# Kernel optimization log

Hardware: AMD Instinct MI355X
Metric: run time of the kernel (lower is better)

Reference implementation:

```python
import jax, jax.numpy as jnp
import numpy as np

HIDDEN = 4096
NUM_HEADS = 32
HEAD_DIM = HIDDEN // NUM_HEADS  # 128
ROPE_THETA = 10000.0
B, S = 1, 2048


def setup_inputs() -> dict:
    key = jax.random.key(0)
    k1, k2, k3, k4 = jax.random.split(key, 4)
    positions = jnp.broadcast_to(jnp.arange(S, dtype=jnp.int32), (B, S))
    hidden_states = jax.random.normal(k1, (B, S, HIDDEN), dtype=jnp.float32)
    # fused QKV projection (bias=True), output projection (bias=False)
    w_qkv = jax.random.normal(k2, (HIDDEN, 3 * HIDDEN), dtype=jnp.float32) * (HIDDEN ** -0.5)
    b_qkv = jax.random.normal(k3, (3 * HIDDEN,), dtype=jnp.float32) * 0.01
    w_o = jax.random.normal(k4, (HIDDEN, HIDDEN), dtype=jnp.float32) * (HIDDEN ** -0.5)
    return {"positions": positions, "hidden_states": hidden_states,
            "w_qkv": w_qkv, "b_qkv": b_qkv, "w_o": w_o}


def _apply_rope(x, positions):
    # x: [B, S, N, D]; NeoX-style rotate-half RoPE, rotary_dim == head_dim
    half = HEAD_DIM // 2
    inv_freq = 1.0 / (ROPE_THETA ** (jnp.arange(0, half, dtype=jnp.float32) / half))
    angles = positions.astype(jnp.float32)[..., None] * inv_freq  # [B, S, half]
    cos = jnp.cos(angles)[:, :, None, :]  # [B, S, 1, half]
    sin = jnp.sin(angles)[:, :, None, :]
    x1, x2 = x[..., :half], x[..., half:]
    return jnp.concatenate([x1 * cos - x2 * sin, x2 * cos + x1 * sin], axis=-1)


def reference(positions, hidden_states, w_qkv, b_qkv, w_o):
    qkv = jnp.einsum('bsh,hd->bsd', hidden_states, w_qkv) + b_qkv  # [B, S, 3H]
    q, k, v = jnp.split(qkv, 3, axis=-1)
    q = q.reshape(B, S, NUM_HEADS, HEAD_DIM)
    k = k.reshape(B, S, NUM_HEADS, HEAD_DIM)
    v = v.reshape(B, S, NUM_HEADS, HEAD_DIM)
    q = _apply_rope(q, positions)
    k = _apply_rope(k, positions)
    scale = HEAD_DIM ** -0.5
    scores = jnp.einsum('bqnd,bknd->bnqk', q, k) * scale  # [B, N, S, S]
    causal = jnp.tril(jnp.ones((S, S), dtype=bool))
    scores = jnp.where(causal, scores, jnp.finfo(scores.dtype).min)
    probs = jax.nn.softmax(scores, axis=-1)
    attn = jnp.einsum('bnqk,bknd->bqnd', probs, v).reshape(B, S, HIDDEN)
    return jnp.einsum('bsh,ho->bso', attn, w_o)
```

## Files before the change

### kernel.cpp

```cpp
#include <hip/hip_runtime.h>
#include <hip/hip_bf16.h>

#define S_LEN 2048
#define HID   4096
#define NH    32
#define HD    128
#define KD    4096

typedef __attribute__((ext_vector_type(4))) float f32x4;
typedef __attribute__((ext_vector_type(8))) short s16x8;
typedef __attribute__((ext_vector_type(4))) short s16x4;

#define AS1 __attribute__((address_space(1)))
#define AS3 __attribute__((address_space(3)))

__device__ __forceinline__ void gl_lds16(const void* g, void* l) {
  __builtin_amdgcn_global_load_lds((const AS1 void*)g, (AS3 void*)l, 16, 0, 0);
}

__device__ inline short f2bf(float f) {
  union { float f; unsigned u; } v; v.f = f;
  return (short)((v.u + 0x7fffu + ((v.u >> 16) & 1u)) >> 16);
}
__device__ inline float bf2f(short s) {
  union { unsigned u; float f; } v; v.u = ((unsigned)(unsigned short)s) << 16;
  return v.f;
}
__device__ inline unsigned packbf(float a, float b) {
  return (unsigned)(unsigned short)f2bf(a) | ((unsigned)(unsigned short)f2bf(b) << 16);
}

__global__ __launch_bounds__(256)
void cvt_kernel(const float* __restrict__ A, short* __restrict__ Ab) {
  const size_t i = ((size_t)blockIdx.x * 256 + threadIdx.x) * 8;
  f32x4 v0 = *(const f32x4*)&A[i];
  f32x4 v1 = *(const f32x4*)&A[i + 4];
  s16x8 r;
  r[0]=f2bf(v0[0]); r[1]=f2bf(v0[1]); r[2]=f2bf(v0[2]); r[3]=f2bf(v0[3]);
  r[4]=f2bf(v1[0]); r[5]=f2bf(v1[1]); r[6]=f2bf(v1[2]); r[7]=f2bf(v1[3]);
  *(s16x8*)&Ab[i] = r;
}

__global__ __launch_bounds__(256)
void transcvt_kernel(const float* __restrict__ W, short* __restrict__ Wt, const int N) {
  __shared__ float tile[64][65];
  const int k0 = blockIdx.x * 64, n0 = blockIdx.y * 64;
  const int t = threadIdx.x;
#pragma unroll
  for (int i = 0; i < 16; ++i) {
    const int e = i * 256 + t;
    const int k = e >> 6, n = e & 63;
    tile[n][k] = W[(size_t)(k0 + k) * N + n0 + n];
  }
  __syncthreads();
  const int nn = t >> 2, ks = (t & 3) * 16;
  s16x8 a, b;
#pragma unroll
  for (int i = 0; i < 8; i++) a[i] = f2bf(tile[nn][ks + i]);
#pragma unroll
  for (int i = 0; i < 8; i++) b[i] = f2bf(tile[nn][ks + 8 + i]);
  *(s16x8*)&Wt[(size_t)(n0 + nn) * KD + k0 + ks]     = a;
  *(s16x8*)&Wt[(size_t)(n0 + nn) * KD + k0 + ks + 8] = b;
}

template<int EPI>
__global__ __launch_bounds__(256, 2)
void gemm5_kernel(const short* __restrict__ A, const short* __restrict__ Bt,
                  const float* __restrict__ bias,
                  short* __restrict__ Qb, short* __restrict__ Kb, short* __restrict__ Vb,
                  float* __restrict__ Cout)
{
  __shared__ char sm[3][24576] __attribute__((aligned(128)));
  const int KD2 = KD * 2;
  const int bid = blockIdx.x;
  const int xcd = bid & 7, idx = bid >> 3;
  const int m0 = (idx & 7) * 256;
  const int n0 = (xcd * ((EPI == 0) ? 12 : 4) + (idx >> 3)) * 128;

  const int t = threadIdx.x, lane = t & 63, c = lane & 15, g = lane >> 4;
  const int w = t >> 6, wr = w >> 1, wc = w & 1;
  const int flip = ((c >> 1) & 7) << 4;
  const int laneA = wr * 8192 + ((c * 64 + g * 16) ^ flip);
  const int laneB = 16384 + wc * 4096 + ((c * 64 + g * 16) ^ flip);

  const char* srcA[4];
  const char* srcB[2];
#pragma unroll
  for (int j = 0; j < 4; ++j) {
    const int la = j * 4096 + t * 16;
    const int ls = la ^ ((la >> 3) & 0x70);
    srcA[j] = (const char*)A + (size_t)(m0 + (ls >> 6)) * KD2 + (ls & 63);
  }
#pragma unroll
  for (int j = 0; j < 2; ++j) {
    const int la = j * 4096 + t * 16;
    const int ls = la ^ ((la >> 3) & 0x70);
    srcB[j] = (const char*)Bt + (size_t)(n0 + (ls >> 6)) * KD2 + (ls & 63);
  }

  f32x4 acc[8][4];
#pragma unroll
  for (int i = 0; i < 8; i++)
#pragma unroll
    for (int j = 0; j < 4; j++) acc[i][j] = (f32x4){0.f, 0.f, 0.f, 0.f};

#define STG(S, H) do {                                        \
    const size_t ko_ = (size_t)(H) * 64;                      \
    gl_lds16(srcA[0] + ko_, sm[S] + t * 16);                  \
    gl_lds16(srcA[1] + ko_, sm[S] + 4096  + t * 16);          \
    gl_lds16(srcA[2] + ko_, sm[S] + 8192  + t * 16);          \
    gl_lds16(srcA[3] + ko_, sm[S] + 12288 + t * 16);          \
    gl_lds16(srcB[0] + ko_, sm[S] + 16384 + t * 16);          \
    gl_lds16(srcB[1] + ko_, sm[S] + 20480 + t * 16);          \
  } while (0)

#define COMP(S) do {                                                       \
    const char* b_ = sm[S];                                                \
    s16x8 a_[8], bb_[4];                                                   \
    _Pragma("unroll")                                                      \
    for (int mi = 0; mi < 8; ++mi) a_[mi] = *(const s16x8*)(b_ + laneA + mi * 1024); \
    _Pragma("unroll")                                                      \
    for (int ni = 0; ni < 4; ++ni) bb_[ni] = *(const s16x8*)(b_ + laneB + ni * 1024); \
    __builtin_amdgcn_s_setprio(1);                                         \
    _Pragma("unroll")                                                      \
    for (int mi = 0; mi < 8; ++mi)                                         \
      _Pragma("unroll")                                                    \
      for (int ni = 0; ni < 4; ++ni)                                       \
        acc[mi][ni] = __builtin_amdgcn_mfma_f32_16x16x32_bf16(a_[mi], bb_[ni], acc[mi][ni], 0, 0, 0); \
    __builtin_amdgcn_s_setprio(0);                                         \
  } while (0)

#define WAIT6 asm volatile("s_waitcnt vmcnt(6)" ::: "memory")
#define WAIT0 asm volatile("s_waitcnt vmcnt(0)" ::: "memory")
#define BARR  do { __builtin_amdgcn_s_barrier(); asm volatile("" ::: "memory"); } while (0)

  STG(0, 0); STG(1, 1);
  for (int j = 0; j < 42; ++j) {
    const int h = 3 * j;
    WAIT6; BARR; STG(2, h + 2); COMP(0);
    WAIT6; BARR; STG(0, h + 3); COMP(1);
    WAIT6; BARR; STG(1, h + 4); COMP(2);
  }
  WAIT6; BARR; COMP(0);
  WAIT0; BARR; COMP(1);

#undef STG
#undef COMP
#undef WAIT6
#undef WAIT0
#undef BARR

  if (EPI == 0) {
#pragma unroll
    for (int ni = 0; ni < 4; ++ni) {
      const int ncol = n0 + wc * 64 + ni * 16 + c;
      const int which = ncol >> 12;
      const int h = (ncol >> 7) & 31;
      const int dcl = ncol & 127;
      short* dst = (which == 0) ? Qb : ((which == 1) ? Kb : Vb);
      const float bv = bias[ncol];
#pragma unroll
      for (int mi = 0; mi < 8; ++mi)
#pragma unroll
        for (int jj = 0; jj < 4; ++jj) {
          const int row = m0 + wr * 128 + mi * 16 + g * 4 + jj;
          dst[((size_t)h * S_LEN + row) * HD + dcl] = f2bf(acc[mi][ni][jj] + bv);
        }
    }
  } else {
#pragma unroll
    for (int ni = 0; ni < 4; ++ni) {
      const int ncol = n0 + wc * 64 + ni * 16 + c;
#pragma unroll
      for (int mi = 0; mi < 8; ++mi)
#pragma unroll
        for (int jj = 0; jj < 4; ++jj) {
          const int row = m0 + wr * 128 + mi * 16 + g * 4 + jj;
          Cout[(size_t)row * HID + ncol] = acc[mi][ni][jj];
        }
    }
  }
}

__global__ __launch_bounds__(256, 3)
void gemm7_kernel(const short* __restrict__ A, const short* __restrict__ Bt,
                  float* __restrict__ Cout)
{
  __shared__ char sm[3][16384] __attribute__((aligned(128)));
  const int KD2 = KD * 2;
  const int bid = blockIdx.x;
  const int xcd = bid & 7, idx = bid >> 3;
  const int m0 = (idx & 15) * 128;
  const int n0 = (xcd * 4 + (idx >> 4)) * 128;

  const int t = threadIdx.x, lane = t & 63, c = lane & 15, g = lane >> 4;
  const int w = t >> 6, wr = w >> 1, wc = w & 1;
  const int flip = ((c >> 1) & 7) << 4;
  const int laneA = wr * 4096 + ((c * 64 + g * 16) ^ flip);
  const int laneB = 8192 + wc * 4096 + ((c * 64 + g * 16) ^ flip);

  const char* srcA[2];
  const char* srcB[2];
#pragma unroll
  for (int j = 0; j < 2; ++j) {
    const int la = j * 4096 + t * 16;
    const int ls = la ^ ((la >> 3) & 0x70);
    srcA[j] = (const char*)A  + (size_t)(m0 + (ls >> 6)) * KD2 + (ls & 63);
    srcB[j] = (const char*)Bt + (size_t)(n0 + (ls >> 6)) * KD2 + (ls & 63);
  }

  f32x4 acc[4][4];
#pragma unroll
  for (int i = 0; i < 4; i++)
#pragma unroll
    for (int j = 0; j < 4; j++) acc[i][j] = (f32x4){0.f, 0.f, 0.f, 0.f};

#define STG7(S, H) do {                                       \
    const size_t ko_ = (size_t)(H) * 64;                      \
    gl_lds16(srcA[0] + ko_, sm[S] + t * 16);                  \
    gl_lds16(srcA[1] + ko_, sm[S] + 4096  + t * 16);          \
    gl_lds16(srcB[0] + ko_, sm[S] + 8192  + t * 16);          \
    gl_lds16(srcB[1] + ko_, sm[S] + 12288 + t * 16);          \
  } while (0)

#define COMP7(S) do {                                                      \
    const char* b_ = sm[S];                                                \
    s16x8 a_[4], bb_[4];                                                   \
    _Pragma("unroll")                                                      \
    for (int mi = 0; mi < 4; ++mi) a_[mi] = *(const s16x8*)(b_ + laneA + mi * 1024); \
    _Pragma("unroll")                                                      \
    for (int ni = 0; ni < 4; ++ni) bb_[ni] = *(const s16x8*)(b_ + laneB + ni * 1024); \
    __builtin_amdgcn_s_setprio(1);                                         \
    _Pragma("unroll")                                                      \
    for (int mi = 0; mi < 4; ++mi)                                         \
      _Pragma("unroll")                                                    \
      for (int ni = 0; ni < 4; ++ni)                                       \
        acc[mi][ni] = __builtin_amdgcn_mfma_f32_16x16x32_bf16(a_[mi], bb_[ni], acc[mi][ni], 0, 0, 0); \
    __builtin_amdgcn_s_setprio(0);                                         \
  } while (0)

#define WAIT4 asm volatile("s_waitcnt vmcnt(4)" ::: "memory")
#define WAIT0 asm volatile("s_waitcnt vmcnt(0)" ::: "memory")
#define BARR  do { __builtin_amdgcn_s_barrier(); asm volatile("" ::: "memory"); } while (0)

  STG7(0, 0); STG7(1, 1);
  for (int j = 0; j < 42; ++j) {
    const int h = 3 * j;
    WAIT4; BARR; STG7(2, h + 2); COMP7(0);
    WAIT4; BARR; STG7(0, h + 3); COMP7(1);
    WAIT4; BARR; STG7(1, h + 4); COMP7(2);
  }
  WAIT4; BARR; COMP7(0);
  WAIT0; BARR; COMP7(1);

#undef STG7
#undef COMP7
#undef WAIT4
#undef WAIT0
#undef BARR

#pragma unroll
  for (int ni = 0; ni < 4; ++ni) {
    const int ncol = n0 + wc * 64 + ni * 16 + c;
#pragma unroll
    for (int mi = 0; mi < 4; ++mi)
#pragma unroll
      for (int jj = 0; jj < 4; ++jj) {
        const int row = m0 + wr * 64 + mi * 16 + g * 4 + jj;
        Cout[(size_t)row * HID + ncol] = acc[mi][ni][jj];
      }
  }
}

template<int EPI, int ABF16>
__global__ __launch_bounds__(256)
void gemm_kernel(const void* __restrict__ Av, const float* __restrict__ B,
                 const float* __restrict__ bias, const int N,
                 short* __restrict__ Qb, short* __restrict__ Kb, short* __restrict__ Vb,
                 float* __restrict__ Cout)
{
  __shared__ short As[128][40];
  __shared__ short Bs[128][40];
  const int m0 = blockIdx.x * 128;
  const int nb = blockIdx.y * 128;
  const int t  = threadIdx.x;
  const int w = t >> 6, lane = t & 63, c = lane & 15, g = lane >> 4;
  const int wm = (w >> 1) * 64, wn = (w & 1) * 64;

  f32x4 acc[4][4];
#pragma unroll
  for (int i = 0; i < 4; i++)
#pragma unroll
    for (int j = 0; j < 4; j++) acc[i][j] = (f32x4){0.f, 0.f, 0.f, 0.f};

  const int ar = t >> 3;
  const int ac = (t & 7) * 4;
  const int bn = t & 127;
  const int bkq = (t >> 7) * 16;

  for (int k0 = 0; k0 < KD; k0 += 32) {
#pragma unroll
    for (int rr = 0; rr < 4; rr++) {
      const int row = rr * 32 + ar;
      if (ABF16) {
        *(s16x4*)&As[row][ac] =
          *(const s16x4*)((const short*)Av + (size_t)(m0 + row) * KD + k0 + ac);
      } else {
        f32x4 v = *(const f32x4*)((const float*)Av + (size_t)(m0 + row) * KD + k0 + ac);
        s16x4 pk;
        pk[0] = f2bf(v[0]); pk[1] = f2bf(v[1]); pk[2] = f2bf(v[2]); pk[3] = f2bf(v[3]);
        *(s16x4*)&As[row][ac] = pk;
      }
    }
    const float* pB = B + (size_t)(k0 + bkq) * N + nb + bn;
    s16x8 b0, b1;
#pragma unroll
    for (int i = 0; i < 8; i++) b0[i] = f2bf(pB[(size_t)i * N]);
#pragma unroll
    for (int i = 0; i < 8; i++) b1[i] = f2bf(pB[(size_t)(i + 8) * N]);
    *(s16x8*)&Bs[bn][bkq]     = b0;
    *(s16x8*)&Bs[bn][bkq + 8] = b1;
    __syncthreads();
    s16x8 af[4], bfr[4];
#pragma unroll
    for (int i = 0; i < 4; i++) af[i]  = *(const s16x8*)&As[wm + i * 16 + c][g * 8];
#pragma unroll
    for (int i = 0; i < 4; i++) bfr[i] = *(const s16x8*)&Bs[wn + i * 16 + c][g * 8];
#pragma unroll
    for (int mi = 0; mi < 4; mi++)
#pragma unroll
      for (int ni = 0; ni < 4; ni++)
        acc[mi][ni] = __builtin_amdgcn_mfma_f32_16x16x32_bf16(af[mi], bfr[ni], acc[mi][ni], 0, 0, 0);
    __syncthreads();
  }

  if (EPI == 0) {
    const int which = nb >> 12;
    const int h = (nb & 4095) >> 7;
    short* dst = (which == 0) ? Qb : ((which == 1) ? Kb : Vb);
#pragma unroll
    for (int ni = 0; ni < 4; ni++) {
      const int d = wn + ni * 16 + c;
      const float bv = bias[nb + d];
#pragma unroll
      for (int mi = 0; mi < 4; mi++)
#pragma unroll
        for (int j = 0; j < 4; j++) {
          const int row = m0 + wm + mi * 16 + g * 4 + j;
          dst[((size_t)h * S_LEN + row) * HD + d] = f2bf(acc[mi][ni][j] + bv);
        }
    }
  } else {
#pragma unroll
    for (int ni = 0; ni < 4; ni++) {
      const int n = nb + wn + ni * 16 + c;
#pragma unroll
      for (int mi = 0; mi < 4; mi++)
#pragma unroll
        for (int j = 0; j < 4; j++) {
          const int row = m0 + wm + mi * 16 + g * 4 + j;
          Cout[(size_t)row * N + n] = acc[mi][ni][j];
        }
    }
  }
}

__global__ void rope_kernel(const int* __restrict__ positions,
                            short* __restrict__ Qb, short* __restrict__ Kb)
{
  const int s = blockIdx.x;
  const int h = blockIdx.y * 4 + threadIdx.y;
  const int d = threadIdx.x;
  const float pos = (float)positions[s];
  const float inv_freq = exp2f(-(float)d * 0.20762050593046014f);
  const float ang = pos * inv_freq;
  float sn, cs;
  sincosf(ang, &sn, &cs);
  const size_t base = ((size_t)h * S_LEN + s) * HD + d;
  const float scale = 0.08838834764831845f;
  float x1 = bf2f(Qb[base]), x2 = bf2f(Qb[base + 64]);
  Qb[base]      = f2bf((x1 * cs - x2 * sn) * scale);
  Qb[base + 64] = f2bf((x2 * cs + x1 * sn) * scale);
  x1 = bf2f(Kb[base]); x2 = bf2f(Kb[base + 64]);
  Kb[base]      = f2bf(x1 * cs - x2 * sn);
  Kb[base + 64] = f2bf(x2 * cs + x1 * sn);
}

__global__ __launch_bounds__(256)
void vtrans_kernel(const short* __restrict__ V, short* __restrict__ Vt)
{
  __shared__ short tile[64][72];
  const int h = blockIdx.z;
  const int s0 = blockIdx.x * 64;
  const int d0 = blockIdx.y * 64;
  const int tx = threadIdx.x & 63, ty = threadIdx.x >> 6;
  for (int r = ty; r < 64; r += 4)
    tile[r][tx] = V[((size_t)h * S_LEN + s0 + r) * HD + d0 + tx];
  __syncthreads();
  for (int r = ty; r < 64; r += 4)
    Vt[((size_t)h * HD + d0 + r) * S_LEN + s0 + tx] = tile[tx][r];
}

__global__ __launch_bounds__(512)
void attn_kernel(const short* __restrict__ Q, const short* __restrict__ Kg,
                 const short* __restrict__ Vtg, short* __restrict__ attn_out)
{
  __shared__ short Ks[2][64][128];
  __shared__ short Vs[2][128][72];
  const int h = blockIdx.y;
  const int ib = blockIdx.x;
  const int q0a = ib * 128;
  const int q0b = (15 - ib) * 128;
  const int nt0 = 2 * ib + 2;
  const int nt1 = 32 - 2 * ib;
  const int t = threadIdx.x;
  const int w = t >> 6, lane = t & 63, c = lane & 15, g = lane >> 4;
  const short* Qh = Q   + (size_t)h * S_LEN * HD;
  const short* Kh = Kg  + (size_t)h * S_LEN * HD;
  const short* Vh = Vtg + (size_t)h * HD * S_LEN;

  const int krow = t >> 4, kch = t & 15;
  const int vrow = t >> 3, vch = t & 7;
  const int ksw = (kch ^ ((krow & 3) | ((krow >> 1) & 4))) * 16;

  const int rbase = (c >> 2) * 8 + (c & 3);
  const int sb = (rbase & 3) | ((rbase >> 1) & 4);
  int koff[4];
#pragma unroll
  for (int di = 0; di < 4; ++di) koff[di] = ((di * 4 + g) ^ sb) * 16;

  const int qga = q0a + w * 16 + c;
  const int qgb = q0b + w * 16 + c;
  s16x8 qfa[4], qfb[4];
#pragma unroll
  for (int di = 0; di < 4; di++) {
    qfa[di] = *(const s16x8*)&Qh[(size_t)qga * HD + di * 32 + g * 8];
    qfb[di] = *(const s16x8*)&Qh[(size_t)qgb * HD + di * 32 + g * 8];
  }

  f32x4 oa[8], ob[8];
#pragma unroll
  for (int dt = 0; dt < 8; dt++) {
    oa[dt] = (f32x4){0.f, 0.f, 0.f, 0.f};
    ob[dt] = (f32x4){0.f, 0.f, 0.f, 0.f};
  }
  float m_a = -3.0e38f, l_a = 0.f, m_b = -3.0e38f, l_b = 0.f;

#define SM_PANEL(SA, SB, SC, SD, QG, FULL, MR, LR, OARR, PB0, PB1) do {        \
    float v_[16];                                                              \
    if (FULL) {                                                                \
      _Pragma("unroll")                                                        \
      for (int j = 0; j < 4; ++j) {                                            \
        v_[j] = SA[j]; v_[4 + j] = SB[j]; v_[8 + j] = SC[j]; v_[12 + j] = SD[j]; \
      }                                                                        \
    } else {                                                                   \
      _Pragma("unroll")                                                        \
      for (int j = 0; j < 4; ++j) {                                            \
        v_[j]      = (kb + 8 * g + j          <= (QG)) ? SA[j] : -__builtin_inff(); \
        v_[4 + j]  = (kb + 8 * g + 4 + j      <= (QG)) ? SB[j] : -__builtin_inff(); \
        v_[8 + j]  = (kb + 32 + 8 * g + j     <= (QG)) ? SC[j] : -__builtin_inff(); \
        v_[12 + j] = (kb + 32 + 8 * g + 4 + j <= (QG)) ? SD[j] : -__builtin_inff(); \
      }                                                                        \
    }                                                                          \
    float mx_ = v_[0];                                                         \
    _Pragma("unroll")                                                          \
    for (int ii = 1; ii < 16; ++ii) mx_ = fmaxf(mx_, v_[ii]);                  \
    mx_ = fmaxf(mx_, __shfl_xor(mx_, 16, 64));                                 \
    mx_ = fmaxf(mx_, __shfl_xor(mx_, 32, 64));                                 \
    const float mn_ = fmaxf(MR, mx_);                                          \
    if (!__all(mn_ - MR <= 8.0f)) {                                            \
      const float al_ = __expf(MR - mn_);                                      \
      LR *= al_;                                                               \
      _Pragma("unroll")                                                        \
      for (int dt = 0; dt < 8; ++dt)                                           \
        _Pragma("unroll")                                                      \
        for (int j = 0; j < 4; ++j) OARR[dt][j] *= al_;                        \
      MR = mn_;                                                                \
    }                                                                          \
    float p_[16], rs_ = 0.f;                                                   \
    _Pragma("unroll")                                                          \
    for (int ii = 0; ii < 16; ++ii) { p_[ii] = __expf(v_[ii] - MR); rs_ += p_[ii]; } \
    rs_ += __shfl_xor(rs_, 16, 64);                                            \
    rs_ += __shfl_xor(rs_, 32, 64);                                            \
    LR += rs_;                                                                 \
    union { s16x8 v8; unsigned u[4]; } pu0_, pu1_;                             \
    pu0_.u[0] = packbf(p_[0], p_[1]);   pu0_.u[1] = packbf(p_[2], p_[3]);      \
    pu0_.u[2] = packbf(p_[4], p_[5]);   pu0_.u[3] = packbf(p_[6], p_[7]);      \
    pu1_.u[0] = packbf(p_[8], p_[9]);   pu1_.u[1] = packbf(p_[10], p_[11]);    \
    pu1_.u[2] = packbf(p_[12], p_[13]); pu1_.u[3] = packbf(p_[14], p_[15]);    \
    PB0 = pu0_.v8; PB1 = pu1_.v8;                                              \
  } while (0)

  {
#pragma unroll
    for (int i = 0; i < 2; ++i) {
      s16x8 gK = *(const s16x8*)&Kh[(size_t)(i * 32 + krow) * HD + kch * 8];
      s16x8 gV = *(const s16x8*)&Vh[(size_t)(i * 64 + vrow) * S_LEN + vch * 8];
      *(s16x8*)((char*)&Ks[0][0][0] + (i * 32 + krow) * 256 + ksw) = gK;
      *(s16x8*)&Vs[0][i * 64 + vrow][vch * 8] = gV;
    }
  }
  __syncthreads();

  for (int kt = 0; kt < nt1; kt++) {
    const int cur = kt & 1;
    const int kb = kt * 64;
    const bool do0 = (kt < nt0);
    s16x8 gK0, gK1, gV0, gV1;
    if (kt + 1 < nt1) {
      gK0 = *(const s16x8*)&Kh[(size_t)(kb + 64 + krow) * HD + kch * 8];
      gK1 = *(const s16x8*)&Kh[(size_t)(kb + 96 + krow) * HD + kch * 8];
      gV0 = *(const s16x8*)&Vh[(size_t)vrow * S_LEN + kb + 64 + vch * 8];
      gV1 = *(const s16x8*)&Vh[(size_t)(64 + vrow) * S_LEN + kb + 64 + vch * 8];
    }
    f32x4 bA = (f32x4){0,0,0,0}, bB = (f32x4){0,0,0,0};
    f32x4 bC = (f32x4){0,0,0,0}, bD = (f32x4){0,0,0,0};
    f32x4 aA = (f32x4){0,0,0,0}, aB = (f32x4){0,0,0,0};
    f32x4 aC = (f32x4){0,0,0,0}, aD = (f32x4){0,0,0,0};
    const char* kbase = (const char*)&Ks[cur][0][0] + rbase * 256;
    __builtin_amdgcn_s_setprio(1);
    if (do0) {
#pragma unroll
      for (int di = 0; di < 4; ++di) {
        const char* p = kbase + koff[di];
        s16x8 kA = *(const s16x8*)(p);
        s16x8 kB = *(const s16x8*)(p + 1024);
        s16x8 kC = *(const s16x8*)(p + 8192);
        s16x8 kD = *(const s16x8*)(p + 9216);
        bA = __builtin_amdgcn_mfma_f32_16x16x32_bf16(kA, qfb[di], bA, 0, 0, 0);
        bB = __builtin_amdgcn_mfma_f32_16x16x32_bf16(kB, qfb[di], bB, 0, 0, 0);
        bC = __builtin_amdgcn_mfma_f32_16x16x32_bf16(kC, qfb[di], bC, 0, 0, 0);
        bD = __builtin_amdgcn_mfma_f32_16x16x32_bf16(kD, qfb[di], bD, 0, 0, 0);
        aA = __builtin_amdgcn_mfma_f32_16x16x32_bf16(kA, qfa[di], aA, 0, 0, 0);
        aB = __builtin_amdgcn_mfma_f32_16x16x32_bf16(kB, qfa[di], aB, 0, 0, 0);
        aC = __builtin_amdgcn_mfma_f32_16x16x32_bf16(kC, qfa[di], aC, 0, 0, 0);
        aD = __builtin_amdgcn_mfma_f32_16x16x32_bf16(kD, qfa[di], aD, 0, 0, 0);
      }
    } else {
#pragma unroll
      for (int di = 0; di < 4; ++di) {
        const char* p = kbase + koff[di];
        s16x8 kA = *(const s16x8*)(p);
        s16x8 kB = *(const s16x8*)(p + 1024);
        s16x8 kC = *(const s16x8*)(p + 8192);
        s16x8 kD = *(const s16x8*)(p + 9216);
        bA = __builtin_amdgcn_mfma_f32_16x16x32_bf16(kA, qfb[di], bA, 0, 0, 0);
        bB = __builtin_amdgcn_mfma_f32_16x16x32_bf16(kB, qfb[di], bB, 0, 0, 0);
        bC = __builtin_amdgcn_mfma_f32_16x16x32_bf16(kC, qfb[di], bC, 0, 0, 0);
        bD = __builtin_amdgcn_mfma_f32_16x16x32_bf16(kD, qfb[di], bD, 0, 0, 0);
      }
    }
    __builtin_amdgcn_s_setprio(0);
    s16x8 pb0, pb1, pa0, pa1;
    const bool fullb = (kb + 64 <= q0b);
    SM_PANEL(bA, bB, bC, bD, qgb, fullb, m_b, l_b, ob, pb0, pb1);
    if (do0) {
      const bool fulla = (kb + 64 <= q0a);
      SM_PANEL(aA, aB, aC, aD, qga, fulla, m_a, l_a, oa, pa0, pa1);
    }
    __builtin_amdgcn_s_setprio(1);
    if (do0) {
#pragma unroll
      for (int dt = 0; dt < 8; dt++) {
        s16x8 vf0 = *(const s16x8*)&Vs[cur][dt * 16 + c][g * 8];
        s16x8 vf1 = *(const s16x8*)&Vs[cur][dt * 16 + c][32 + g * 8];
        ob[dt] = __builtin_amdgcn_mfma_f32_16x16x32_bf16(vf0, pb0, ob[dt], 0, 0, 0);
        ob[dt] = __builtin_amdgcn_mfma_f32_16x16x32_bf16(vf1, pb1, ob[dt], 0, 0, 0);
        oa[dt] = __builtin_amdgcn_mfma_f32_16x16x32_bf16(vf0, pa0, oa[dt], 0, 0, 0);
        oa[dt] = __builtin_amdgcn_mfma_f32_16x16x32_bf16(vf1, pa1, oa[dt], 0, 0, 0);
      }
    } else {
#pragma unroll
      for (int dt = 0; dt < 8; dt++) {
        s16x8 vf0 = *(const s16x8*)&Vs[cur][dt * 16 + c][g * 8];
        s16x8 vf1 = *(const s16x8*)&Vs[cur][dt * 16 + c][32 + g * 8];
        ob[dt] = __builtin_amdgcn_mfma_f32_16x16x32_bf16(vf0, pb0, ob[dt], 0, 0, 0);
        ob[dt] = __builtin_amdgcn_mfma_f32_16x16x32_bf16(vf1, pb1, ob[dt], 0, 0, 0);
      }
    }
    __builtin_amdgcn_s_setprio(0);
    __syncthreads();
    if (kt + 1 < nt1) {
      *(s16x8*)((char*)&Ks[cur ^ 1][0][0] + krow * 256 + ksw)        = gK0;
      *(s16x8*)((char*)&Ks[cur ^ 1][0][0] + (32 + krow) * 256 + ksw) = gK1;
      *(s16x8*)&Vs[cur ^ 1][vrow][vch * 8]      = gV0;
      *(s16x8*)&Vs[cur ^ 1][64 + vrow][vch * 8] = gV1;
    }
    __syncthreads();
  }
#undef SM_PANEL

  const float inv_b = 1.0f / l_b;
  const float inv_a = 1.0f / l_a;
#pragma unroll
  for (int dt = 0; dt < 8; dt++) {
    s16x4 pkb, pka;
#pragma unroll
    for (int j = 0; j < 4; j++) {
      pkb[j] = f2bf(ob[dt][j] * inv_b);
      pka[j] = f2bf(oa[dt][j] * inv_a);
    }
    *(s16x4*)&attn_out[(size_t)qgb * HID + h * HD + dt * 16 + g * 4] = pkb;
    *(s16x4*)&attn_out[(size_t)qga * HID + h * HD + dt * 16 + g * 4] = pka;
  }
}

extern "C" void kernel_launch(void* const* d_in, const int* in_sizes, int n_in,
                              void* d_out, int out_size, void* d_ws, size_t ws_size,
                              hipStream_t stream)
{
  const int*   positions = (const int*)d_in[0];
  const float* hidden    = (const float*)d_in[1];
  const float* w_qkv     = (const float*)d_in[2];
  const float* b_qkv     = (const float*)d_in[3];
  const float* w_o       = (const float*)d_in[4];
  float* out = (float*)d_out;

  char* ws = (char*)d_ws;
  const size_t MB = (size_t)1 << 20;

  if (ws_size >= 224 * MB) {
    short* Ah    = (short*)(ws);
    short* Wqt   = (short*)(ws + 16 * MB);
    short* Wot   = (short*)(ws + 112 * MB);
    short* Qb    = (short*)(ws + 144 * MB);
    short* Kb    = (short*)(ws + 160 * MB);
    short* Vb    = (short*)(ws + 176 * MB);
    short* Vt    = (short*)(ws + 192 * MB);
    short* attnb = (short*)(ws + 208 * MB);

    cvt_kernel<<<4096, 256, 0, stream>>>(hidden, Ah);
    transcvt_kernel<<<dim3(KD / 64, 3 * HID / 64), 256, 0, stream>>>(w_qkv, Wqt, 3 * HID);
    transcvt_kernel<<<dim3(KD / 64, HID / 64), 256, 0, stream>>>(w_o, Wot, HID);
    gemm5_kernel<0><<<768, 256, 0, stream>>>(Ah, Wqt, b_qkv, Qb, Kb, Vb, nullptr);
    rope_kernel<<<dim3(S_LEN, NH / 4), dim3(64, 4), 0, stream>>>(positions, Qb, Kb);
    vtrans_kernel<<<dim3(S_LEN / 64, HD / 64, NH), 256, 0, stream>>>(Vb, Vt);
    attn_kernel<<<dim3(8, NH), 512, 0, stream>>>(Qb, Kb, Vt, attnb);
    gemm7_kernel<<<512, 256, 0, stream>>>(attnb, Wot, out);
  } else {
    short* Qb    = (short*)(ws);
    short* Kb    = (short*)(ws + 16 * MB);
    short* Vb    = (short*)(ws + 32 * MB);
    short* Vt    = (short*)(ws + 48 * MB);
    short* attnb = (short*)(ws + 64 * MB);

    gemm_kernel<0, 0><<<dim3(16, 96), 256, 0, stream>>>(hidden, w_qkv, b_qkv, 3 * HID,
                                                        Qb, Kb, Vb, nullptr);
    rope_kernel<<<dim3(S_LEN, NH / 4), dim3(64, 4), 0, stream>>>(positions, Qb, Kb);
    vtrans_kernel<<<dim3(S_LEN / 64, HD / 64, NH), 256, 0, stream>>>(Vb, Vt);
    attn_kernel<<<dim3(8, NH), 512, 0, stream>>>(Qb, Kb, Vt, attnb);
    gemm_kernel<1, 1><<<dim3(16, 32), 256, 0, stream>>>(attnb, w_o, nullptr, HID,
                                                        nullptr, nullptr, nullptr, out);
  }
}
```

Before: 469.8 us.

## Split GEMM k-step into two half-phases with interleaved staging and barriers

```diff
diff --git a/kernel.cpp b/kernel.cpp
--- a/kernel.cpp
+++ b/kernel.cpp
@@ -65,7 +65,7 @@
 
 template<int EPI>
 __global__ __launch_bounds__(256, 2)
-void gemm5_kernel(const short* __restrict__ A, const short* __restrict__ Bt,
+void gemm8_kernel(const short* __restrict__ A, const short* __restrict__ Bt,
                   const float* __restrict__ bias,
                   short* __restrict__ Qb, short* __restrict__ Kb, short* __restrict__ Vb,
                   float* __restrict__ Cout)
@@ -104,51 +104,66 @@
 #pragma unroll
     for (int j = 0; j < 4; j++) acc[i][j] = (f32x4){0.f, 0.f, 0.f, 0.f};
 
-#define STG(S, H) do {                                        \
+#define STG_H1(S, H) do {                                     \
     const size_t ko_ = (size_t)(H) * 64;                      \
     gl_lds16(srcA[0] + ko_, sm[S] + t * 16);                  \
     gl_lds16(srcA[1] + ko_, sm[S] + 4096  + t * 16);          \
     gl_lds16(srcA[2] + ko_, sm[S] + 8192  + t * 16);          \
+  } while (0)
+#define STG_H2(S, H) do {                                     \
+    const size_t ko_ = (size_t)(H) * 64;                      \
     gl_lds16(srcA[3] + ko_, sm[S] + 12288 + t * 16);          \
     gl_lds16(srcB[0] + ko_, sm[S] + 16384 + t * 16);          \
     gl_lds16(srcB[1] + ko_, sm[S] + 20480 + t * 16);          \
   } while (0)
 
-#define COMP(S) do {                                                       \
+#define TILE8(S, S2, H, DOSTG, WN) do {                                    \
+    asm volatile("s_waitcnt vmcnt(" #WN ")" ::: "memory");                 \
+    __builtin_amdgcn_s_barrier();                                          \
+    if (DOSTG) STG_H1(S2, H);                                              \
     const char* b_ = sm[S];                                                \
-    s16x8 a_[8], bb_[4];                                                   \
+    s16x8 al_[4], bb_[4];                                                  \
     _Pragma("unroll")                                                      \
-    for (int mi = 0; mi < 8; ++mi) a_[mi] = *(const s16x8*)(b_ + laneA + mi * 1024); \
+    for (int mi = 0; mi < 4; ++mi) al_[mi] = *(const s16x8*)(b_ + laneA + mi * 1024); \
     _Pragma("unroll")                                                      \
     for (int ni = 0; ni < 4; ++ni) bb_[ni] = *(const s16x8*)(b_ + laneB + ni * 1024); \
+    __builtin_amdgcn_s_barrier();                                          \
     __builtin_amdgcn_s_setprio(1);                                         \
     _Pragma("unroll")                                                      \
-    for (int mi = 0; mi < 8; ++mi)                                         \
+    for (int mi = 0; mi < 4; ++mi)                                         \
       _Pragma("unroll")                                                    \
       for (int ni = 0; ni < 4; ++ni)                                       \
-        acc[mi][ni] = __builtin_amdgcn_mfma_f32_16x16x32_bf16(a_[mi], bb_[ni], acc[mi][ni], 0, 0, 0); \
+        acc[mi][ni] = __builtin_amdgcn_mfma_f32_16x16x32_bf16(al_[mi], bb_[ni], acc[mi][ni], 0, 0, 0); \
+    __builtin_amdgcn_s_setprio(0);                                         \
+    __builtin_amdgcn_s_barrier();                                          \
+    if (DOSTG) STG_H2(S2, H);                                              \
+    s16x8 ah_[4];                                                          \
+    _Pragma("unroll")                                                      \
+    for (int mi = 0; mi < 4; ++mi) ah_[mi] = *(const s16x8*)(b_ + laneA + (4 + mi) * 1024); \
+    __builtin_amdgcn_s_barrier();                                          \
+    __builtin_amdgcn_s_setprio(1);                                         \
+    _Pragma("unroll")                                                      \
+    for (int mi = 0; mi < 4; ++mi)                                         \
+      _Pragma("unroll")                                                    \
+      for (int ni = 0; ni < 4; ++ni)                                       \
+        acc[4 + mi][ni] = __builtin_amdgcn_mfma_f32_16x16x32_bf16(ah_[mi], bb_[ni], acc[4 + mi][ni], 0, 0, 0); \
     __builtin_amdgcn_s_setprio(0);                                         \
   } while (0)
 
-#define WAIT6 asm volatile("s_waitcnt vmcnt(6)" ::: "memory")
-#define WAIT0 asm volatile("s_waitcnt vmcnt(0)" ::: "memory")
-#define BARR  do { __builtin_amdgcn_s_barrier(); asm volatile("" ::: "memory"); } while (0)
-
-  STG(0, 0); STG(1, 1);
+  STG_H1(0, 0); STG_H2(0, 0);
+  STG_H1(1, 1); STG_H2(1, 1);
   for (int j = 0; j < 42; ++j) {
     const int h = 3 * j;
-    WAIT6; BARR; STG(2, h + 2); COMP(0);
-    WAIT6; BARR; STG(0, h + 3); COMP(1);
-    WAIT6; BARR; STG(1, h + 4); COMP(2);
-  }
-  WAIT6; BARR; COMP(0);
-  WAIT0; BARR; COMP(1);
-
-#undef STG
-#undef COMP
-#undef WAIT6
-#undef WAIT0
-#undef BARR
+    TILE8(0, 2, h + 2, true, 6);
+    TILE8(1, 0, h + 3, true, 6);
+    TILE8(2, 1, h + 4, true, 6);
+  }
+  TILE8(0, 0, 0, false, 6);
+  TILE8(1, 0, 0, false, 0);
+
+#undef STG_H1
+#undef STG_H2
+#undef TILE8
 
   if (EPI == 0) {
 #pragma unroll
@@ -179,96 +194,6 @@
           Cout[(size_t)row * HID + ncol] = acc[mi][ni][jj];
         }
     }
-  }
-}
-
-__global__ __launch_bounds__(256, 3)
-void gemm7_kernel(const short* __restrict__ A, const short* __restrict__ Bt,
-                  float* __restrict__ Cout)
-{
-  __shared__ char sm[3][16384] __attribute__((aligned(128)));
-  const int KD2 = KD * 2;
-  const int bid = blockIdx.x;
-  const int xcd = bid & 7, idx = bid >> 3;
-  const int m0 = (idx & 15) * 128;
-  const int n0 = (xcd * 4 + (idx >> 4)) * 128;
-
-  const int t = threadIdx.x, lane = t & 63, c = lane & 15, g = lane >> 4;
-  const int w = t >> 6, wr = w >> 1, wc = w & 1;
-  const int flip = ((c >> 1) & 7) << 4;
-  const int laneA = wr * 4096 + ((c * 64 + g * 16) ^ flip);
-  const int laneB = 8192 + wc * 4096 + ((c * 64 + g * 16) ^ flip);
-
-  const char* srcA[2];
-  const char* srcB[2];
-#pragma unroll
-  for (int j = 0; j < 2; ++j) {
-    const int la = j * 4096 + t * 16;
-    const int ls = la ^ ((la >> 3) & 0x70);
-    srcA[j] = (const char*)A  + (size_t)(m0 + (ls >> 6)) * KD2 + (ls & 63);
-    srcB[j] = (const char*)Bt + (size_t)(n0 + (ls >> 6)) * KD2 + (ls & 63);
-  }
-
-  f32x4 acc[4][4];
-#pragma unroll
-  for (int i = 0; i < 4; i++)
-#pragma unroll
-    for (int j = 0; j < 4; j++) acc[i][j] = (f32x4){0.f, 0.f, 0.f, 0.f};
-
-#define STG7(S, H) do {                                       \
-    const size_t ko_ = (size_t)(H) * 64;                      \
-    gl_lds16(srcA[0] + ko_, sm[S] + t * 16);                  \
-    gl_lds16(srcA[1] + ko_, sm[S] + 4096  + t * 16);          \
-    gl_lds16(srcB[0] + ko_, sm[S] + 8192  + t * 16);          \
-    gl_lds16(srcB[1] + ko_, sm[S] + 12288 + t * 16);          \
-  } while (0)
-
-#define COMP7(S) do {                                                      \
-    const char* b_ = sm[S];                                                \
-    s16x8 a_[4], bb_[4];                                                   \
-    _Pragma("unroll")                                                      \
-    for (int mi = 0; mi < 4; ++mi) a_[mi] = *(const s16x8*)(b_ + laneA + mi * 1024); \
-    _Pragma("unroll")                                                      \
-    for (int ni = 0; ni < 4; ++ni) bb_[ni] = *(const s16x8*)(b_ + laneB + ni * 1024); \
-    __builtin_amdgcn_s_setprio(1);                                         \
-    _Pragma("unroll")                                                      \
-    for (int mi = 0; mi < 4; ++mi)                                         \
-      _Pragma("unroll")                                                    \
-      for (int ni = 0; ni < 4; ++ni)                                       \
-        acc[mi][ni] = __builtin_amdgcn_mfma_f32_16x16x32_bf16(a_[mi], bb_[ni], acc[mi][ni], 0, 0, 0); \
-    __builtin_amdgcn_s_setprio(0);                                         \
-  } while (0)
-
-#define WAIT4 asm volatile("s_waitcnt vmcnt(4)" ::: "memory")
-#define WAIT0 asm volatile("s_waitcnt vmcnt(0)" ::: "memory")
-#define BARR  do { __builtin_amdgcn_s_barrier(); asm volatile("" ::: "memory"); } while (0)
-
-  STG7(0, 0); STG7(1, 1);
-  for (int j = 0; j < 42; ++j) {
-    const int h = 3 * j;
-    WAIT4; BARR; STG7(2, h + 2); COMP7(0);
-    WAIT4; BARR; STG7(0, h + 3); COMP7(1);
-    WAIT4; BARR; STG7(1, h + 4); COMP7(2);
-  }
-  WAIT4; BARR; COMP7(0);
-  WAIT0; BARR; COMP7(1);
-
-#undef STG7
-#undef COMP7
-#undef WAIT4
-#undef WAIT0
-#undef BARR
-
-#pragma unroll
-  for (int ni = 0; ni < 4; ++ni) {
-    const int ncol = n0 + wc * 64 + ni * 16 + c;
-#pragma unroll
-    for (int mi = 0; mi < 4; ++mi)
-#pragma unroll
-      for (int jj = 0; jj < 4; ++jj) {
-        const int row = m0 + wr * 64 + mi * 16 + g * 4 + jj;
-        Cout[(size_t)row * HID + ncol] = acc[mi][ni][jj];
-      }
   }
 }
 
@@ -632,11 +557,12 @@
     cvt_kernel<<<4096, 256, 0, stream>>>(hidden, Ah);
     transcvt_kernel<<<dim3(KD / 64, 3 * HID / 64), 256, 0, stream>>>(w_qkv, Wqt, 3 * HID);
     transcvt_kernel<<<dim3(KD / 64, HID / 64), 256, 0, stream>>>(w_o, Wot, HID);
-    gemm5_kernel<0><<<768, 256, 0, stream>>>(Ah, Wqt, b_qkv, Qb, Kb, Vb, nullptr);
+    gemm8_kernel<0><<<768, 256, 0, stream>>>(Ah, Wqt, b_qkv, Qb, Kb, Vb, nullptr);
     rope_kernel<<<dim3(S_LEN, NH / 4), dim3(64, 4), 0, stream>>>(positions, Qb, Kb);
     vtrans_kernel<<<dim3(S_LEN / 64, HD / 64, NH), 256, 0, stream>>>(Vb, Vt);
     attn_kernel<<<dim3(8, NH), 512, 0, stream>>>(Qb, Kb, Vt, attnb);
-    gemm7_kernel<<<512, 256, 0, stream>>>(attnb, Wot, out);
+    gemm8_kernel<1><<<256, 256, 0, stream>>>(attnb, Wot, nullptr,
+                                             nullptr, nullptr, nullptr, out);
   } else {
     short* Qb    = (short*)(ws);
     short* Kb    = (short*)(ws + 16 * MB);
```

Result: no change. 467.5 us (-0.5%).
